# Performance work log

Measured on AMD Instinct MI355X. Metric: run time of the kernel, lower is better.

The kernel has to match this reference:

```python
import jax, jax.numpy as jnp
import numpy as np

L, B, S, D, N, H = 4, 4, 1024, 1024, 64, 16   # layers, batch, seq, d_model, d_state, heads
DI = 2 * D      # d_inner (expand_factor=2)
DH = D // H     # head dim
DF = 4 * D      # ffn hidden
SCALE = 1.0 / np.sqrt(DH)


def setup_inputs() -> dict:
    key = jax.random.key(0)
    ks = jax.random.split(key, 12)
    w = lambda k, sh: jax.random.normal(k, sh, jnp.float32) * 0.02
    return {
        "x": jax.random.normal(ks[0], (B, S, D), jnp.float32),
        "A_log": jax.random.normal(ks[1], (L, N), jnp.float32),
        "Dp": jax.random.normal(ks[2], (L, D), jnp.float32),
        "W_in": w(ks[3], (L, 2 * DI, D)), "b_in": jnp.zeros((L, 2 * DI), jnp.float32),
        "W_xp": w(ks[4], (L, N, DI)), "b_xp": jnp.zeros((L, N), jnp.float32),
        "W_dt": w(ks[5], (L, D, DI)), "b_dt": jnp.zeros((L, D), jnp.float32),
        "W_out": w(ks[6], (L, D, DI)), "b_out": jnp.zeros((L, D), jnp.float32),
        "W_qkv": w(ks[7], (L, 3 * D, D)), "b_qkv": jnp.zeros((L, 3 * D), jnp.float32),
        "W_ao": w(ks[8], (L, D, D)), "b_ao": jnp.zeros((L, D), jnp.float32),
        "g1": jnp.ones((L, D), jnp.float32), "be1": jnp.zeros((L, D), jnp.float32),
        "g2": jnp.ones((L, D), jnp.float32), "be2": jnp.zeros((L, D), jnp.float32),
        "W_f1": w(ks[9], (L, DF, D)), "b_f1": jnp.zeros((L, DF), jnp.float32),
        "W_f2": w(ks[10], (L, D, DF)), "b_f2": jnp.zeros((L, D), jnp.float32),
    }


def _ln(x, g, b, eps=1e-5):
    mu = x.mean(-1, keepdims=True)
    var = ((x - mu) ** 2).mean(-1, keepdims=True)
    return (x - mu) * jax.lax.rsqrt(var + eps) * g + b


def _mamba(x, A_log, Dp, W_in, b_in, W_xp, b_xp, W_dt, b_dt, W_out, b_out):
    xr = jnp.einsum('bsd,od->bso', x, W_in) + b_in          # [b,s,2*DI]
    xi, res = jnp.split(xr, 2, axis=-1)
    xi = jax.nn.silu(xi)
    A = -jnp.exp(A_log)                                      # [N]
    delta = jax.nn.softplus(jnp.einsum('bsi,di->bsd', xi, W_dt) + b_dt)  # [b,s,D]
    m = delta.mean(-1)                                       # [b,s]
    A_disc = jnp.exp(A[None, None, :] * m[:, :, None])       # [b,s,N]
    u = jnp.einsum('bsi,ni->bsn', xi, W_xp) + b_xp           # [b,s,N]

    def step(state, inp):
        a_t, u_t = inp
        state = a_t * state + u_t                            # [b,N]
        return state, state.sum(-1)                          # carry, emit sum over d_state

    init = jnp.zeros((x.shape[0], A_log.shape[0]), x.dtype)
    _, ssum = jax.lax.scan(step, init, (A_disc.swapaxes(0, 1), u.swapaxes(0, 1)))
    ssum = ssum.swapaxes(0, 1)                               # [b,s]
    y = ssum[..., None] * xi                                 # [b,s,DI]
    y = y * jax.nn.silu(res)
    y = jnp.einsum('bsi,di->bsd', y, W_out) + b_out
    return y + x * Dp


def _attn(x, W_qkv, b_qkv, W_ao, b_ao):
    b, s, d = x.shape
    qkv = jnp.einsum('bsd,od->bso', x, W_qkv) + b_qkv        # [b,s,3d]
    qkv = qkv.reshape(b, s, 3, H, DH)
    q = jnp.moveaxis(qkv[:, :, 0], 2, 1)                     # [b,h,s,dh]
    k = jnp.moveaxis(qkv[:, :, 1], 2, 1)
    v = jnp.moveaxis(qkv[:, :, 2], 2, 1)
    scores = jnp.einsum('bhqd,bhkd->bhqk', q, k) * SCALE
    wts = jax.nn.softmax(scores, axis=-1)
    o = jnp.einsum('bhqk,bhkd->bhqd', wts, v)
    o = jnp.moveaxis(o, 1, 2).reshape(b, s, d)
    return jnp.einsum('bsd,od->bso', o, W_ao) + b_ao


def _forward(x, A_log, Dp, W_in, b_in, W_xp, b_xp, W_dt, b_dt, W_out, b_out,
             W_qkv, b_qkv, W_ao, b_ao, g1, be1, g2, be2, W_f1, b_f1, W_f2, b_f2):
    for l in range(L):
        m = _mamba(x, A_log[l], Dp[l], W_in[l], b_in[l], W_xp[l], b_xp[l],
                   W_dt[l], b_dt[l], W_out[l], b_out[l])
        x = _ln(x + m, g1[l], be1[l])
        a = _attn(x, W_qkv[l], b_qkv[l], W_ao[l], b_ao[l])
        x = _ln(x + a, g2[l], be2[l])
        h = jax.nn.gelu(jnp.einsum('bsd,fd->bsf', x, W_f1[l]) + b_f1[l], approximate=False)
        x = x + jnp.einsum('bsf,df->bsd', h, W_f2[l]) + b_f2[l]
    return x


def reference(x, A_log, Dp, W_in, b_in, W_xp, b_xp, W_dt, b_dt, W_out, b_out,
              W_qkv, b_qkv, W_ao, b_ao, g1, be1, g2, be2, W_f1, b_f1, W_f2, b_f2):
    return _forward(x, A_log, Dp, W_in, b_in, W_xp, b_xp, W_dt, b_dt, W_out, b_out,
                    W_qkv, b_qkv, W_ao, b_ao, g1, be1, g2, be2, W_f1, b_f1, W_f2, b_f2)
```

## Files before the change

kernel.cpp:

```cpp
#include <hip/hip_runtime.h>
#include <math.h>

typedef unsigned short ushort_t;
typedef unsigned int uint_t;
typedef __attribute__((ext_vector_type(8))) short short8;
typedef __attribute__((ext_vector_type(4))) float f32x4;

constexpr int Bb = 4, Ss = 1024, Dd = 1024, Nn = 64, Hh = 16;
constexpr int DIi = 2048, DFf = 4096;
constexpr int TOKENS = Bb * Ss;

constexpr size_t O_IN  = 0;
constexpr size_t O_DT  = 4194304;
constexpr size_t O_XP  = O_DT + 2097152;
constexpr size_t O_OUT = O_XP + 262144;
constexpr size_t O_QKV = O_OUT + 2097152;
constexpr size_t O_AO  = O_QKV + 3145728;
constexpr size_t O_F1  = O_AO + 1048576;
constexpr size_t O_F2  = O_F1 + 4194304;
constexpr size_t W_TOTAL = O_F2 + 4194304;
constexpr size_t W_QUADS = W_TOTAL / 4;

enum { EPI_SPLIT = 0, EPI_B16, EPI_GELU, EPI_DTXP, EPI_DP, EPI_F32, EPI_RESID };

__device__ __forceinline__ float siluf(float x) { return x / (1.f + expf(-x)); }
__device__ __forceinline__ float softplusf(float x) { return fmaxf(x, 0.f) + log1pf(expf(-fabsf(x))); }
__device__ __forceinline__ float geluf(float x) { return 0.5f * x * (1.f + erff(x * 0.7071067811865476f)); }

__device__ __forceinline__ float bf2f(uint_t u) {
    union { uint_t i; float f; } v; v.i = u << 16; return v.f;
}
__device__ __forceinline__ ushort_t f2bf(float f) {
    union { float f; uint_t i; } v; v.f = f;
    return (ushort_t)((v.i + 0x7FFFu + ((v.i >> 16) & 1u)) >> 16);
}

__device__ __forceinline__ void gload_lds16(const ushort_t* g, ushort_t* l) {
    __builtin_amdgcn_global_load_lds(
        (const __attribute__((address_space(1))) unsigned int*)g,
        (__attribute__((address_space(3))) unsigned int*)l, 16, 0, 0);
}

template <int EPI>
__global__ __launch_bounds__(256) void gemm_mfma(
    const ushort_t* __restrict__ A, const ushort_t* __restrict__ Bw,
    const float* __restrict__ bias, int M, int N, int K,
    float* __restrict__ of0, float* __restrict__ of1,
    ushort_t* __restrict__ ob0, ushort_t* __restrict__ ob1,
    const float* __restrict__ e0, const float* __restrict__ e1)
{
    __shared__ __attribute__((aligned(16))) ushort_t AB[24576];
    const int tid = threadIdx.x;
    const int lane = tid & 63, wid = tid >> 6;
    const int wr = wid >> 1, wc = wid & 1;
    const int l15 = lane & 15, lg = lane >> 4;

    int bx = blockIdx.x, by = blockIdx.y;
    const int gx = gridDim.x;
    if ((gx & 7) == 0) {
        const int s = by * gx + bx;
        const int xcd = s & 7, c = s >> 3;
        const int cpx = gx >> 3;
        bx = xcd * cpx + (c % cpx);
        by = c / cpx;
    }
    const int m0 = by << 7, n0 = bx << 7;

    f32x4 acc[4][4];
#pragma unroll
    for (int i = 0; i < 4; ++i)
#pragma unroll
        for (int j = 0; j < 4; ++j) { acc[i][j][0] = 0.f; acc[i][j][1] = 0.f; acc[i][j][2] = 0.f; acc[i][j][3] = 0.f; }

    const int srow4 = lane >> 2;
    const int scc4  = (lane & 3) ^ ((lane >> 3) & 3);
    const ushort_t* Ag = A + (size_t)(m0 + wid * 32 + srow4) * K + scc4 * 8;
    const ushort_t* Bg = Bw + (size_t)(n0 + wid * 32 + srow4) * K + scc4 * 8;

#define STAGE_(b_, k0_)                                                          \
    {                                                                            \
        ushort_t* d_ = AB + (b_) * 8192;                                         \
        gload_lds16(Ag + (k0_),                  d_ + (wid * 32) * 32);          \
        gload_lds16(Ag + (size_t)16 * K + (k0_), d_ + (wid * 32 + 16) * 32);     \
        gload_lds16(Bg + (k0_),                  d_ + 4096 + (wid * 32) * 32);   \
        gload_lds16(Bg + (size_t)16 * K + (k0_), d_ + 4096 + (wid * 32 + 16) * 32); \
    }

    const int NS = K >> 5;
    STAGE_(0, 0);
    STAGE_(1, 32);
    asm volatile("s_waitcnt vmcnt(4)" ::: "memory");
    __builtin_amdgcn_s_barrier();

    const int chAB = (lg ^ ((l15 >> 1) & 3)) * 8;
    int bc = 0, bp = 2;
    for (int s = 0; s < NS; ++s) {
        if (s + 2 < NS) STAGE_(bp, (s + 2) << 5);
        const ushort_t* As_ = AB + bc * 8192;
        const ushort_t* Bs_ = As_ + 4096;
        short8 af[4], bfr[4];
#pragma unroll
        for (int mi = 0; mi < 4; ++mi)
            af[mi] = *(const short8*)&As_[(wr * 64 + mi * 16 + l15) * 32 + chAB];
#pragma unroll
        for (int nj = 0; nj < 4; ++nj)
            bfr[nj] = *(const short8*)&Bs_[(wc * 64 + nj * 16 + l15) * 32 + chAB];
#pragma unroll
        for (int mi = 0; mi < 4; ++mi)
#pragma unroll
            for (int nj = 0; nj < 4; ++nj)
                acc[mi][nj] = __builtin_amdgcn_mfma_f32_16x16x32_bf16(
                    af[mi], bfr[nj], acc[mi][nj], 0, 0, 0);
        if (s + 1 < NS) {
            if (s + 2 < NS) asm volatile("s_waitcnt vmcnt(4)" ::: "memory");
            else            asm volatile("s_waitcnt vmcnt(0)" ::: "memory");
            __builtin_amdgcn_s_barrier();
        }
        bc = (bc == 2) ? 0 : bc + 1;
        bp = (bp == 2) ? 0 : bp + 1;
    }
#undef STAGE_
    __syncthreads();

    if (EPI == EPI_SPLIT || EPI == EPI_B16 || EPI == EPI_GELU) {
        const bool lo = (EPI != EPI_SPLIT) || (n0 < DIi);
#pragma unroll
        for (int nj = 0; nj < 4; ++nj) {
            const int coll = wc * 64 + nj * 16 + l15;
            const float bv = bias[n0 + coll];
#pragma unroll
            for (int mi = 0; mi < 4; ++mi)
#pragma unroll
                for (int r = 0; r < 4; ++r) {
                    float v = acc[mi][nj][r] + bv;
                    if (EPI == EPI_SPLIT) v = lo ? siluf(v) : v;
                    else if (EPI == EPI_GELU) v = geluf(v);
                    AB[(wr * 64 + mi * 16 + lg * 4 + r) * 128 + coll] = f2bf(v);
                }
        }
        __syncthreads();
        ushort_t* dst = (EPI == EPI_SPLIT) ? (lo ? ob0 : ob1) : ob0;
        const int Nd = (EPI == EPI_SPLIT) ? DIi : N;
        const int nb = (EPI == EPI_SPLIT && !lo) ? (n0 - DIi) : n0;
#pragma unroll
        for (int i = 0; i < 8; ++i) {
            const int c = i * 256 + tid;
            const int row = c >> 4, ch = c & 15;
            *(uint4*)&dst[(size_t)(m0 + row) * Nd + nb + ch * 8] =
                *(const uint4*)&AB[row * 128 + ch * 8];
        }
    } else {
        float* Cf = (float*)AB;
#pragma unroll
        for (int pass = 0; pass < 2; ++pass) {
            if (pass) __syncthreads();
            if (wr == pass) {
#pragma unroll
                for (int nj = 0; nj < 4; ++nj) {
                    const int coll = wc * 64 + nj * 16 + l15;
                    const float bv = bias[n0 + coll];
#pragma unroll
                    for (int mi = 0; mi < 4; ++mi)
#pragma unroll
                        for (int r = 0; r < 4; ++r)
                            Cf[(mi * 16 + lg * 4 + r) * 128 + coll] = acc[mi][nj][r] + bv;
                }
            }
            __syncthreads();
#pragma unroll
            for (int i = 0; i < 8; ++i) {
                const int c = i * 256 + tid;
                const int row = c >> 5, ch = c & 31;
                const int grow = m0 + pass * 64 + row;
                const int gcol = n0 + ch * 4;
                float4 v = *(const float4*)&Cf[row * 128 + ch * 4];
                if (EPI == EPI_DTXP) {
                    if (n0 < Dd) {
                        v.x = softplusf(v.x); v.y = softplusf(v.y);
                        v.z = softplusf(v.z); v.w = softplusf(v.w);
                        *(float4*)&of0[(size_t)grow * Dd + gcol] = v;
                    } else {
                        *(float4*)&of1[(size_t)grow * 128 + (gcol - Dd)] = v;
                    }
                } else if (EPI == EPI_DP) {
                    const float4 e = *(const float4*)&e0[(size_t)grow * N + gcol];
                    const float4 d = *(const float4*)&e1[gcol];
                    v.x = fmaf(e.x, d.x, v.x); v.y = fmaf(e.y, d.y, v.y);
                    v.z = fmaf(e.z, d.z, v.z); v.w = fmaf(e.w, d.w, v.w);
                    *(float4*)&of0[(size_t)grow * N + gcol] = v;
                } else if (EPI == EPI_F32) {
                    *(float4*)&of0[(size_t)grow * N + gcol] = v;
                } else {
                    const float4 e = *(const float4*)&e0[(size_t)grow * N + gcol];
                    v.x += e.x; v.y += e.y; v.z += e.z; v.w += e.w;
                    *(float4*)&of0[(size_t)grow * N + gcol] = v;
                    uint2 w;
                    w.x = (uint_t)f2bf(v.x) | ((uint_t)f2bf(v.y) << 16);
                    w.y = (uint_t)f2bf(v.z) | ((uint_t)f2bf(v.w) << 16);
                    *(uint2*)&ob0[(size_t)grow * N + gcol] = w;
                }
            }
        }
    }
}

__global__ __launch_bounds__(256) void convert_weights_kernel(
    const float* __restrict__ Win, const float* __restrict__ Wdt,
    const float* __restrict__ Wxp, const float* __restrict__ Wout,
    const float* __restrict__ Wqkv, const float* __restrict__ Wao,
    const float* __restrict__ Wf1, const float* __restrict__ Wf2,
    const float* __restrict__ bdt, const float* __restrict__ bxp,
    ushort_t* __restrict__ dst, float* __restrict__ bcat)
{
    size_t q = (size_t)blockIdx.x * blockDim.x + threadIdx.x;
    if (q < 288) {
#pragma unroll
        for (int j = 0; j < 4; ++j) {
            const int e = (int)q * 4 + j;
            bcat[e] = (e < Dd) ? bdt[e] : ((e < Dd + Nn) ? bxp[e - Dd] : 0.f);
        }
    }
    const size_t stride = (size_t)gridDim.x * blockDim.x;
    for (; q < W_QUADS; q += stride) {
        const size_t e = q * 4;
        float4 v;
        if (e < O_DT)       v = *(const float4*)&Win[e - O_IN];
        else if (e < O_XP)  v = *(const float4*)&Wdt[e - O_DT];
        else if (e < O_OUT) {
            const size_t li = e - O_XP;
            const int row = (int)(li >> 11), colq = (int)(li & 2047);
            v = (row < Nn) ? *(const float4*)&Wxp[(size_t)row * DIi + colq]
                           : make_float4(0.f, 0.f, 0.f, 0.f);
        }
        else if (e < O_QKV) v = *(const float4*)&Wout[e - O_OUT];
        else if (e < O_AO)  v = *(const float4*)&Wqkv[e - O_QKV];
        else if (e < O_F1)  v = *(const float4*)&Wao[e - O_AO];
        else if (e < O_F2)  v = *(const float4*)&Wf1[e - O_F1];
        else                v = *(const float4*)&Wf2[e - O_F2];
        uint2 w;
        w.x = (uint_t)f2bf(v.x) | ((uint_t)f2bf(v.y) << 16);
        w.y = (uint_t)f2bf(v.z) | ((uint_t)f2bf(v.w) << 16);
        *(uint2*)&dst[e] = w;
    }
}

__global__ __launch_bounds__(256) void cvt_f32_bf16_kernel(
    const float* __restrict__ in, ushort_t* __restrict__ out)
{
    const size_t i4 = (size_t)blockIdx.x * blockDim.x + threadIdx.x;
    const float4 v = *(const float4*)&in[i4 * 4];
    uint2 w;
    w.x = (uint_t)f2bf(v.x) | ((uint_t)f2bf(v.y) << 16);
    w.y = (uint_t)f2bf(v.z) | ((uint_t)f2bf(v.w) << 16);
    *(uint2*)&out[i4 * 4] = w;
}

__global__ __launch_bounds__(256) void row_mean_kernel(const float* __restrict__ in,
                                                       float* __restrict__ out)
{
    __shared__ float red[4];
    const int tid = threadIdx.x;
    const size_t base = (size_t)blockIdx.x * Dd;
    const float4 v = *(const float4*)&in[base + tid * 4];
    float s = v.x + v.y + v.z + v.w;
#pragma unroll
    for (int off = 32; off; off >>= 1) s += __shfl_xor(s, off);
    if ((tid & 63) == 0) red[tid >> 6] = s;
    __syncthreads();
    if (tid == 0) out[blockIdx.x] = (red[0] + red[1] + red[2] + red[3]) * (1.f / (float)Dd);
}

__global__ __launch_bounds__(256) void ln_residual_kernel(
    float* __restrict__ xio, const float* __restrict__ addin,
    const float* __restrict__ g, const float* __restrict__ be,
    ushort_t* __restrict__ xb)
{
    __shared__ float red[8];
    const int tid = threadIdx.x;
    const size_t base = (size_t)blockIdx.x * Dd;
    const float4 xv = *(const float4*)&xio[base + tid * 4];
    const float4 av = *(const float4*)&addin[base + tid * 4];
    float v[4] = {xv.x + av.x, xv.y + av.y, xv.z + av.z, xv.w + av.w};
    float s = v[0] + v[1] + v[2] + v[3];
    float s2 = v[0] * v[0] + v[1] * v[1] + v[2] * v[2] + v[3] * v[3];
#pragma unroll
    for (int off = 32; off; off >>= 1) { s += __shfl_xor(s, off); s2 += __shfl_xor(s2, off); }
    if ((tid & 63) == 0) { red[tid >> 6] = s; red[4 + (tid >> 6)] = s2; }
    __syncthreads();
    const float mu = (red[0] + red[1] + red[2] + red[3]) * (1.f / (float)Dd);
    const float var = (red[4] + red[5] + red[6] + red[7]) * (1.f / (float)Dd) - mu * mu;
    const float rstd = rsqrtf(var + 1e-5f);
    const float4 gv = *(const float4*)&g[tid * 4];
    const float4 bv = *(const float4*)&be[tid * 4];
    float o[4];
    o[0] = (v[0] - mu) * rstd * gv.x + bv.x;
    o[1] = (v[1] - mu) * rstd * gv.y + bv.y;
    o[2] = (v[2] - mu) * rstd * gv.z + bv.z;
    o[3] = (v[3] - mu) * rstd * gv.w + bv.w;
    *(float4*)&xio[base + tid * 4] = make_float4(o[0], o[1], o[2], o[3]);
    uint2 w;
    w.x = (uint_t)f2bf(o[0]) | ((uint_t)f2bf(o[1]) << 16);
    w.y = (uint_t)f2bf(o[2]) | ((uint_t)f2bf(o[3]) << 16);
    *(uint2*)&xb[base + tid * 4] = w;
}

__global__ __launch_bounds__(1024) void scan_fused_kernel(
    const float* __restrict__ A_log_l, const float* __restrict__ m,
    const float* __restrict__ u, float* __restrict__ ssum)
{
    __shared__ float Ps[16][64];
    __shared__ float Sl[16][64];
    __shared__ float Cs[16][64];
    const int b = blockIdx.x;
    const int tid = threadIdx.x;
    const int n = tid & 63, c = tid >> 6;
    const int t0 = b * Ss + c * 64;
    const float Aval = -expf(A_log_l[n]);

    float S = 0.f, msum = 0.f;
#pragma unroll 8
    for (int t = 0; t < 64; ++t) {
        const float mt = m[t0 + t];
        msum += mt;
        S = fmaf(expf(Aval * mt), S, u[(size_t)(t0 + t) * 128 + n]);
    }
    Ps[c][n] = expf(Aval * msum);
    Sl[c][n] = S;
    __syncthreads();

    if (c == 0) {
        float carry = 0.f;
#pragma unroll
        for (int cc = 0; cc < 16; ++cc) {
            Cs[cc][n] = carry;
            carry = fmaf(Ps[cc][n], carry, Sl[cc][n]);
        }
    }
    __syncthreads();

    float st = Cs[c][n];
#pragma unroll 4
    for (int t = 0; t < 64; ++t) {
        st = fmaf(expf(Aval * m[t0 + t]), st, u[(size_t)(t0 + t) * 128 + n]);
        float r = st;
#pragma unroll
        for (int off = 32; off; off >>= 1) r += __shfl_xor(r, off);
        if (n == 0) ssum[t0 + t] = r;
    }
}

__global__ __launch_bounds__(256) void y_gate_kernel(
    ushort_t* __restrict__ xi, const ushort_t* __restrict__ res,
    const float* __restrict__ ssum)
{
    const size_t i8 = (size_t)blockIdx.x * blockDim.x + threadIdx.x;
    const int t = (int)(i8 >> 8);
    const float sv = ssum[t];
    uint4 xw = *(const uint4*)&xi[i8 * 8];
    const uint4 rw = *(const uint4*)&res[i8 * 8];
    const uint_t xs[4] = {xw.x, xw.y, xw.z, xw.w};
    const uint_t rs[4] = {rw.x, rw.y, rw.z, rw.w};
    uint_t os[4];
#pragma unroll
    for (int j = 0; j < 4; ++j) {
        const float x0 = bf2f(xs[j] & 0xffffu), x1 = bf2f(xs[j] >> 16);
        const float r0 = bf2f(rs[j] & 0xffffu), r1 = bf2f(rs[j] >> 16);
        os[j] = (uint_t)f2bf(sv * x0 * siluf(r0)) | ((uint_t)f2bf(sv * x1 * siluf(r1)) << 16);
    }
    *(uint4*)&xi[i8 * 8] = make_uint4(os[0], os[1], os[2], os[3]);
}

__global__ __launch_bounds__(256) void transpose_v_kernel(
    const ushort_t* __restrict__ qkv, ushort_t* __restrict__ vt)
{
    __shared__ ushort_t T[64][68];
    const int b = blockIdx.z, h = blockIdx.y, st = blockIdx.x;
    const int tid = threadIdx.x;
    const int sl = tid >> 3, d0 = (tid & 7) * 8;
#pragma unroll
    for (int it = 0; it < 2; ++it) {
        const int s = sl + it * 32;
        const uint4 w = *(const uint4*)&qkv[(size_t)(b * Ss + st * 64 + s) * 3072 + 2048 + h * 64 + d0];
        *(uint2*)&T[s][d0]     = make_uint2(w.x, w.y);
        *(uint2*)&T[s][d0 + 4] = make_uint2(w.z, w.w);
    }
    __syncthreads();
    const int dl = tid >> 3, s0 = (tid & 7) * 8;
#pragma unroll
    for (int it = 0; it < 2; ++it) {
        const int d = dl + it * 32;
        uint_t w[4];
#pragma unroll
        for (int j = 0; j < 4; ++j)
            w[j] = (uint_t)T[s0 + 2 * j][d] | ((uint_t)T[s0 + 2 * j + 1][d] << 16);
        *(uint4*)&vt[(size_t)((b * Hh + h) * 64 + d) * Ss + st * 64 + s0] =
            make_uint4(w[0], w[1], w[2], w[3]);
    }
}

__global__ __launch_bounds__(256) void attn_mfma_kernel(
    const ushort_t* __restrict__ qkv, const ushort_t* __restrict__ vt,
    ushort_t* __restrict__ out)
{
    __shared__ ushort_t Ks[64 * 64];
    __shared__ ushort_t Vs[64 * 64];
    __shared__ __attribute__((aligned(16))) ushort_t Pb[4][2560];

    const int tid = threadIdx.x;
    const int lane = tid & 63, wid = tid >> 6;
    const int b = blockIdx.z, h = blockIdx.y;
    const int q0 = blockIdx.x * 128 + wid * 32;
    const int l15 = lane & 15, lg = lane >> 4;
    constexpr float CEXP = 0.125f * 1.44269504f;

    short8 qf[2][2];
#pragma unroll
    for (int mi = 0; mi < 2; ++mi)
#pragma unroll
        for (int kk = 0; kk < 2; ++kk)
            qf[mi][kk] = *(const short8*)&qkv[(size_t)(b * Ss + q0 + mi * 16 + l15) * 3072
                                              + h * 64 + kk * 32 + lg * 8];

    f32x4 oacc[2][4];
#pragma unroll
    for (int mi = 0; mi < 2; ++mi)
#pragma unroll
        for (int nj = 0; nj < 4; ++nj) { oacc[mi][nj][0]=0.f; oacc[mi][nj][1]=0.f; oacc[mi][nj][2]=0.f; oacc[mi][nj][3]=0.f; }
    float lrun[2][4];
#pragma unroll
    for (int mi = 0; mi < 2; ++mi)
#pragma unroll
        for (int r = 0; r < 4; ++r) lrun[mi][r] = 0.f;

    const int srow = lane >> 3;
    const int scc  = (lane & 7) ^ srow;
    const ushort_t* Kg = qkv + (size_t)(b * Ss + wid * 16 + srow) * 3072 + 1024 + h * 64 + scc * 8;
    const ushort_t* Vg = vt + (size_t)((b * Hh + h) * 64 + wid * 16 + srow) * Ss + scc * 8;

    for (int kt = 0; kt < Ss / 64; ++kt) {
#pragma unroll
        for (int j = 0; j < 2; ++j) {
            gload_lds16(Kg + (size_t)(kt * 64 + j * 8) * 3072, Ks + (wid * 16 + j * 8) * 64);
            gload_lds16(Vg + (size_t)j * 8 * Ss + kt * 64,     Vs + (wid * 16 + j * 8) * 64);
        }
        __syncthreads();

        f32x4 sacc[2][4];
#pragma unroll
        for (int mi = 0; mi < 2; ++mi)
#pragma unroll
            for (int nj = 0; nj < 4; ++nj) { sacc[mi][nj][0]=0.f; sacc[mi][nj][1]=0.f; sacc[mi][nj][2]=0.f; sacc[mi][nj][3]=0.f; }
#pragma unroll
        for (int kk = 0; kk < 2; ++kk) {
            short8 kf[4];
#pragma unroll
            for (int nj = 0; nj < 4; ++nj) {
                const int row = nj * 16 + l15;
                const int ch = (kk * 4 + lg) ^ (row & 7);
                kf[nj] = *(const short8*)&Ks[row * 64 + ch * 8];
            }
#pragma unroll
            for (int mi = 0; mi < 2; ++mi)
#pragma unroll
                for (int nj = 0; nj < 4; ++nj)
                    sacc[mi][nj] = __builtin_amdgcn_mfma_f32_16x16x32_bf16(
                        qf[mi][kk], kf[nj], sacc[mi][nj], 0, 0, 0);
        }

#pragma unroll
        for (int mi = 0; mi < 2; ++mi)
#pragma unroll
            for (int nj = 0; nj < 4; ++nj) {
                const int bi = mi * 2 + (nj >> 1);
                const int chsw = ((nj & 1) * 2 + (l15 >> 3)) ^ lg;
#pragma unroll
                for (int r = 0; r < 4; ++r) {
                    const float p = exp2f(sacc[mi][nj][r] * CEXP);
                    lrun[mi][r] += p;
                    const int q15 = lg * 4 + r;
                    Pb[wid][bi * 640 + q15 * 40 + chsw * 8 + (lane & 7)] = f2bf(p);
                }
            }

#pragma unroll
        for (int kk = 0; kk < 2; ++kk) {
            short8 pa[2], vb[4];
#pragma unroll
            for (int mi = 0; mi < 2; ++mi) {
                const int chsw = lg ^ (l15 >> 2);
                pa[mi] = *(const short8*)&Pb[wid][(mi * 2 + kk) * 640 + l15 * 40 + chsw * 8];
            }
#pragma unroll
            for (int nj = 0; nj < 4; ++nj) {
                const int row = nj * 16 + l15;
                const int ch = (kk * 4 + lg) ^ (row & 7);
                vb[nj] = *(const short8*)&Vs[row * 64 + ch * 8];
            }
#pragma unroll
            for (int mi = 0; mi < 2; ++mi)
#pragma unroll
                for (int nj = 0; nj < 4; ++nj)
                    oacc[mi][nj] = __builtin_amdgcn_mfma_f32_16x16x32_bf16(
                        pa[mi], vb[nj], oacc[mi][nj], 0, 0, 0);
        }
        __syncthreads();
    }

#pragma unroll
    for (int mi = 0; mi < 2; ++mi)
#pragma unroll
        for (int r = 0; r < 4; ++r) {
            float s = lrun[mi][r];
#pragma unroll
            for (int off = 1; off < 16; off <<= 1) s += __shfl_xor(s, off);
            lrun[mi][r] = 1.f / s;
        }
#pragma unroll
    for (int mi = 0; mi < 2; ++mi)
#pragma unroll
        for (int r = 0; r < 4; ++r) {
            const int q = q0 + mi * 16 + lg * 4 + r;
            const float inv = lrun[mi][r];
#pragma unroll
            for (int nj = 0; nj < 4; ++nj)
                out[(size_t)(b * Ss + q) * Dd + h * 64 + nj * 16 + l15] =
                    f2bf(oacc[mi][nj][r] * inv);
        }
}

extern "C" void kernel_launch(void* const* d_in, const int* in_sizes, int n_in,
                              void* d_out, int out_size, void* d_ws, size_t ws_size,
                              hipStream_t stream)
{
    const float* x_in  = (const float*)d_in[0];
    const float* A_log = (const float*)d_in[1];
    const float* Dp    = (const float*)d_in[2];
    const float* W_in  = (const float*)d_in[3];
    const float* b_in  = (const float*)d_in[4];
    const float* W_xp  = (const float*)d_in[5];
    const float* b_xp  = (const float*)d_in[6];
    const float* W_dt  = (const float*)d_in[7];
    const float* b_dt  = (const float*)d_in[8];
    const float* W_out = (const float*)d_in[9];
    const float* b_out = (const float*)d_in[10];
    const float* W_qkv = (const float*)d_in[11];
    const float* b_qkv = (const float*)d_in[12];
    const float* W_ao  = (const float*)d_in[13];
    const float* b_ao  = (const float*)d_in[14];
    const float* g1    = (const float*)d_in[15];
    const float* be1   = (const float*)d_in[16];
    const float* g2    = (const float*)d_in[17];
    const float* be2   = (const float*)d_in[18];
    const float* W_f1  = (const float*)d_in[19];
    const float* b_f1  = (const float*)d_in[20];
    const float* W_f2  = (const float*)d_in[21];
    const float* b_f2  = (const float*)d_in[22];

    float* xf      = (float*)d_ws;
    float* a3      = xf + 4194304;
    float* ub      = a3 + 4194304;
    float* mb      = ub + 524288;
    float* sb      = mb + 4096;
    float* bcat    = sb + 4096;
    ushort_t* xb    = (ushort_t*)(bcat + 1152);
    ushort_t* xi_b  = xb + 4194304;
    ushort_t* res_b = xi_b + 8388608;
    ushort_t* qh_b  = res_b + 8388608;
    ushort_t* ao_b  = qh_b + 16777216;
    ushort_t* Wb    = ao_b + 4194304;
    ushort_t* vt_b  = Wb + W_TOTAL;

    hipMemcpyAsync(xf, x_in, (size_t)TOKENS * Dd * sizeof(float),
                   hipMemcpyDeviceToDevice, stream);
    cvt_f32_bf16_kernel<<<dim3(4096), dim3(256), 0, stream>>>(x_in, xb);

    const dim3 blk(256);

    for (int l = 0; l < 4; ++l) {
        convert_weights_kernel<<<dim3(2048), blk, 0, stream>>>(
            W_in + (size_t)l * 4194304, W_dt + (size_t)l * 2097152,
            W_xp + (size_t)l * 131072,  W_out + (size_t)l * 2097152,
            W_qkv + (size_t)l * 3145728, W_ao + (size_t)l * 1048576,
            W_f1 + (size_t)l * 4194304, W_f2 + (size_t)l * 4194304,
            b_dt + (size_t)l * 1024, b_xp + (size_t)l * Nn, Wb, bcat);

        gemm_mfma<EPI_SPLIT><<<dim3(32, 32), blk, 0, stream>>>(
            xb, Wb + O_IN, b_in + (size_t)l * 4096, TOKENS, 4096, 1024,
            nullptr, nullptr, xi_b, res_b, nullptr, nullptr);
        gemm_mfma<EPI_DTXP><<<dim3(9, 32), blk, 0, stream>>>(
            xi_b, Wb + O_DT, bcat, TOKENS, 1152, 2048,
            a3, ub, nullptr, nullptr, nullptr, nullptr);
        row_mean_kernel<<<dim3(TOKENS), blk, 0, stream>>>(a3, mb);
        scan_fused_kernel<<<dim3(Bb), dim3(1024), 0, stream>>>(
            A_log + (size_t)l * Nn, mb, ub, sb);
        y_gate_kernel<<<dim3(4096), blk, 0, stream>>>(xi_b, res_b, sb);
        gemm_mfma<EPI_DP><<<dim3(8, 32), blk, 0, stream>>>(
            xi_b, Wb + O_OUT, b_out + (size_t)l * 1024, TOKENS, 1024, 2048,
            a3, nullptr, nullptr, nullptr, xf, Dp + (size_t)l * 1024);
        ln_residual_kernel<<<dim3(TOKENS), blk, 0, stream>>>(
            xf, a3, g1 + (size_t)l * 1024, be1 + (size_t)l * 1024, xb);
        gemm_mfma<EPI_B16><<<dim3(24, 32), blk, 0, stream>>>(
            xb, Wb + O_QKV, b_qkv + (size_t)l * 3072, TOKENS, 3072, 1024,
            nullptr, nullptr, qh_b, nullptr, nullptr, nullptr);
        transpose_v_kernel<<<dim3(16, Hh, Bb), blk, 0, stream>>>(qh_b, vt_b);
        attn_mfma_kernel<<<dim3(8, Hh, Bb), blk, 0, stream>>>(qh_b, vt_b, ao_b);
        gemm_mfma<EPI_F32><<<dim3(8, 32), blk, 0, stream>>>(
            ao_b, Wb + O_AO, b_ao + (size_t)l * 1024, TOKENS, 1024, 1024,
            a3, nullptr, nullptr, nullptr, nullptr, nullptr);
        ln_residual_kernel<<<dim3(TOKENS), blk, 0, stream>>>(
            xf, a3, g2 + (size_t)l * 1024, be2 + (size_t)l * 1024, xb);
        gemm_mfma<EPI_GELU><<<dim3(32, 32), blk, 0, stream>>>(
            xb, Wb + O_F1, b_f1 + (size_t)l * 4096, TOKENS, 4096, 1024,
            nullptr, nullptr, qh_b, nullptr, nullptr, nullptr);
        gemm_mfma<EPI_RESID><<<dim3(8, 32), blk, 0, stream>>>(
            qh_b, Wb + O_F2, b_f2 + (size_t)l * 1024, TOKENS, 1024, 4096,
            xf, nullptr, xb, nullptr, xf, nullptr);
    }

    hipMemcpyAsync(d_out, xf, (size_t)TOKENS * Dd * sizeof(float),
                   hipMemcpyDeviceToDevice, stream);
    (void)in_sizes; (void)n_in; (void)out_size; (void)ws_size;
}
```

Measured before the change: 1.890 ms.

## Add 64-row GEMM tiles for narrow outputs and deepen LDS pipeline

Templates the GEMM on an M tile size and a buffer count. The narrow-N GEMMs (dt/xp, out-proj, attn-out, FFN2) switch to 64x128 tiles with 4 waves side by side along N, which doubles grid size from 256-288 blocks so the many CUs on the chip stay busy. Most GEMMs also move from a 3-buffer to a 4-buffer global-to-LDS prefetch with a generalized vmcnt wait. The smaller tiles cut data reuse per block, and the deeper buffering raises LDS use, which may lower occupancy.

```diff
diff --git a/kernel.cpp b/kernel.cpp
--- a/kernel.cpp
+++ b/kernel.cpp
@@ -41,7 +41,15 @@
         (__attribute__((address_space(3))) unsigned int*)l, 16, 0, 0);
 }
 
-template <int EPI>
+__device__ __forceinline__ void wait_vm(int n) {
+    if (n == 0)      asm volatile("s_waitcnt vmcnt(0)" ::: "memory");
+    else if (n == 3) asm volatile("s_waitcnt vmcnt(3)" ::: "memory");
+    else if (n == 4) asm volatile("s_waitcnt vmcnt(4)" ::: "memory");
+    else if (n == 6) asm volatile("s_waitcnt vmcnt(6)" ::: "memory");
+    else             asm volatile("s_waitcnt vmcnt(8)" ::: "memory");
+}
+
+template <int EPI, int MT, int NBUF>
 __global__ __launch_bounds__(256) void gemm_mfma(
     const ushort_t* __restrict__ A, const ushort_t* __restrict__ Bw,
     const float* __restrict__ bias, int M, int N, int K,
@@ -49,10 +57,16 @@
     ushort_t* __restrict__ ob0, ushort_t* __restrict__ ob1,
     const float* __restrict__ e0, const float* __restrict__ e1)
 {
-    __shared__ __attribute__((aligned(16))) ushort_t AB[24576];
+    constexpr int BUFSZ = (MT == 128) ? 8192 : 6144;
+    constexpr int DEPTH = NBUF - 1;
+    constexpr int L     = (MT == 128) ? 4 : 3;
+    constexpr int NJ    = (MT == 128) ? 4 : 2;
+    __shared__ __attribute__((aligned(16))) ushort_t AB[NBUF * BUFSZ];
+
     const int tid = threadIdx.x;
     const int lane = tid & 63, wid = tid >> 6;
-    const int wr = wid >> 1, wc = wid & 1;
+    const int wr = (MT == 128) ? (wid >> 1) : 0;
+    const int wc = (MT == 128) ? (wid & 1) : wid;
     const int l15 = lane & 15, lg = lane >> 4;
 
     int bx = blockIdx.x, by = blockIdx.y;
@@ -64,65 +78,82 @@
         bx = xcd * cpx + (c % cpx);
         by = c / cpx;
     }
-    const int m0 = by << 7, n0 = bx << 7;
-
-    f32x4 acc[4][4];
+    const int m0 = by * MT, n0 = bx << 7;
+
+    f32x4 acc[4][NJ];
 #pragma unroll
     for (int i = 0; i < 4; ++i)
 #pragma unroll
-        for (int j = 0; j < 4; ++j) { acc[i][j][0] = 0.f; acc[i][j][1] = 0.f; acc[i][j][2] = 0.f; acc[i][j][3] = 0.f; }
+        for (int j = 0; j < NJ; ++j) { acc[i][j][0] = 0.f; acc[i][j][1] = 0.f; acc[i][j][2] = 0.f; acc[i][j][3] = 0.f; }
 
     const int srow4 = lane >> 2;
     const int scc4  = (lane & 3) ^ ((lane >> 3) & 3);
     const ushort_t* Ag = A + (size_t)(m0 + wid * 32 + srow4) * K + scc4 * 8;
     const ushort_t* Bg = Bw + (size_t)(n0 + wid * 32 + srow4) * K + scc4 * 8;
-
-#define STAGE_(b_, k0_)                                                          \
-    {                                                                            \
-        ushort_t* d_ = AB + (b_) * 8192;                                         \
-        gload_lds16(Ag + (k0_),                  d_ + (wid * 32) * 32);          \
-        gload_lds16(Ag + (size_t)16 * K + (k0_), d_ + (wid * 32 + 16) * 32);     \
-        gload_lds16(Bg + (k0_),                  d_ + 4096 + (wid * 32) * 32);   \
-        gload_lds16(Bg + (size_t)16 * K + (k0_), d_ + 4096 + (wid * 32 + 16) * 32); \
-    }
+    const ushort_t* sb64[3];
+    int do64[3];
+    if (MT == 64) {
+#pragma unroll
+        for (int j = 0; j < 3; ++j) {
+            const int i = wid * 3 + j;
+            const bool isA = i < 4;
+            const int rb = (isA ? i : i - 4) * 16;
+            sb64[j] = (isA ? A + (size_t)(m0 + rb + srow4) * K
+                           : Bw + (size_t)(n0 + rb + srow4) * K) + scc4 * 8;
+            do64[j] = (isA ? 0 : 2048) + rb * 32;
+        }
+    }
+
+    auto STAGE = [&](int b_, int k0_) {
+        ushort_t* d_ = AB + b_ * BUFSZ;
+        if constexpr (MT == 128) {
+            gload_lds16(Ag + k0_,                  d_ + (wid * 32) * 32);
+            gload_lds16(Ag + (size_t)16 * K + k0_, d_ + (wid * 32 + 16) * 32);
+            gload_lds16(Bg + k0_,                  d_ + 4096 + (wid * 32) * 32);
+            gload_lds16(Bg + (size_t)16 * K + k0_, d_ + 4096 + (wid * 32 + 16) * 32);
+        } else {
+#pragma unroll
+            for (int j = 0; j < 3; ++j)
+                gload_lds16(sb64[j] + k0_, d_ + do64[j]);
+        }
+    };
 
     const int NS = K >> 5;
-    STAGE_(0, 0);
-    STAGE_(1, 32);
-    asm volatile("s_waitcnt vmcnt(4)" ::: "memory");
+#pragma unroll
+    for (int p = 0; p < DEPTH; ++p) STAGE(p, p * 32);
+    wait_vm((DEPTH - 1) * L);
     __builtin_amdgcn_s_barrier();
 
     const int chAB = (lg ^ ((l15 >> 1) & 3)) * 8;
-    int bc = 0, bp = 2;
+    int bc = 0, bp = DEPTH;
     for (int s = 0; s < NS; ++s) {
-        if (s + 2 < NS) STAGE_(bp, (s + 2) << 5);
-        const ushort_t* As_ = AB + bc * 8192;
-        const ushort_t* Bs_ = As_ + 4096;
-        short8 af[4], bfr[4];
+        if (s + DEPTH < NS) STAGE(bp, (s + DEPTH) << 5);
+        const ushort_t* As_ = AB + bc * BUFSZ;
+        const ushort_t* Bs_ = As_ + ((MT == 128) ? 4096 : 2048);
+        short8 af[4], bfr[NJ];
 #pragma unroll
         for (int mi = 0; mi < 4; ++mi)
             af[mi] = *(const short8*)&As_[(wr * 64 + mi * 16 + l15) * 32 + chAB];
 #pragma unroll
-        for (int nj = 0; nj < 4; ++nj)
-            bfr[nj] = *(const short8*)&Bs_[(wc * 64 + nj * 16 + l15) * 32 + chAB];
+        for (int nj = 0; nj < NJ; ++nj)
+            bfr[nj] = *(const short8*)&Bs_[(wc * (MT == 128 ? 64 : 32) + nj * 16 + l15) * 32 + chAB];
 #pragma unroll
         for (int mi = 0; mi < 4; ++mi)
 #pragma unroll
-            for (int nj = 0; nj < 4; ++nj)
+            for (int nj = 0; nj < NJ; ++nj)
                 acc[mi][nj] = __builtin_amdgcn_mfma_f32_16x16x32_bf16(
                     af[mi], bfr[nj], acc[mi][nj], 0, 0, 0);
         if (s + 1 < NS) {
-            if (s + 2 < NS) asm volatile("s_waitcnt vmcnt(4)" ::: "memory");
-            else            asm volatile("s_waitcnt vmcnt(0)" ::: "memory");
+            const int rem = NS - 2 - s;
+            wait_vm(((rem < DEPTH - 1) ? rem : DEPTH - 1) * L);
             __builtin_amdgcn_s_barrier();
         }
-        bc = (bc == 2) ? 0 : bc + 1;
-        bp = (bp == 2) ? 0 : bp + 1;
-    }
-#undef STAGE_
+        bc = (bc + 1 == NBUF) ? 0 : bc + 1;
+        bp = (bp + 1 == NBUF) ? 0 : bp + 1;
+    }
     __syncthreads();
 
-    if (EPI == EPI_SPLIT || EPI == EPI_B16 || EPI == EPI_GELU) {
+    if constexpr (MT == 128) {
         const bool lo = (EPI != EPI_SPLIT) || (n0 < DIi);
 #pragma unroll
         for (int nj = 0; nj < 4; ++nj) {
@@ -152,53 +183,47 @@
     } else {
         float* Cf = (float*)AB;
 #pragma unroll
-        for (int pass = 0; pass < 2; ++pass) {
-            if (pass) __syncthreads();
-            if (wr == pass) {
-#pragma unroll
-                for (int nj = 0; nj < 4; ++nj) {
-                    const int coll = wc * 64 + nj * 16 + l15;
-                    const float bv = bias[n0 + coll];
-#pragma unroll
-                    for (int mi = 0; mi < 4; ++mi)
-#pragma unroll
-                        for (int r = 0; r < 4; ++r)
-                            Cf[(mi * 16 + lg * 4 + r) * 128 + coll] = acc[mi][nj][r] + bv;
+        for (int nj = 0; nj < NJ; ++nj) {
+            const int coll = wc * 32 + nj * 16 + l15;
+            const float bv = bias[n0 + coll];
+#pragma unroll
+            for (int mi = 0; mi < 4; ++mi)
+#pragma unroll
+                for (int r = 0; r < 4; ++r)
+                    Cf[(mi * 16 + lg * 4 + r) * 128 + coll] = acc[mi][nj][r] + bv;
+        }
+        __syncthreads();
+#pragma unroll
+        for (int i = 0; i < 8; ++i) {
+            const int c = i * 256 + tid;
+            const int row = c >> 5, ch = c & 31;
+            const int grow = m0 + row;
+            const int gcol = n0 + ch * 4;
+            float4 v = *(const float4*)&Cf[row * 128 + ch * 4];
+            if (EPI == EPI_DTXP) {
+                if (n0 < Dd) {
+                    v.x = softplusf(v.x); v.y = softplusf(v.y);
+                    v.z = softplusf(v.z); v.w = softplusf(v.w);
+                    *(float4*)&of0[(size_t)grow * Dd + gcol] = v;
+                } else {
+                    *(float4*)&of1[(size_t)grow * 128 + (gcol - Dd)] = v;
                 }
-            }
-            __syncthreads();
-#pragma unroll
-            for (int i = 0; i < 8; ++i) {
-                const int c = i * 256 + tid;
-                const int row = c >> 5, ch = c & 31;
-                const int grow = m0 + pass * 64 + row;
-                const int gcol = n0 + ch * 4;
-                float4 v = *(const float4*)&Cf[row * 128 + ch * 4];
-                if (EPI == EPI_DTXP) {
-                    if (n0 < Dd) {
-                        v.x = softplusf(v.x); v.y = softplusf(v.y);
-                        v.z = softplusf(v.z); v.w = softplusf(v.w);
-                        *(float4*)&of0[(size_t)grow * Dd + gcol] = v;
-                    } else {
-                        *(float4*)&of1[(size_t)grow * 128 + (gcol - Dd)] = v;
-                    }
-                } else if (EPI == EPI_DP) {
-                    const float4 e = *(const float4*)&e0[(size_t)grow * N + gcol];
-                    const float4 d = *(const float4*)&e1[gcol];
-                    v.x = fmaf(e.x, d.x, v.x); v.y = fmaf(e.y, d.y, v.y);
-                    v.z = fmaf(e.z, d.z, v.z); v.w = fmaf(e.w, d.w, v.w);
-                    *(float4*)&of0[(size_t)grow * N + gcol] = v;
-                } else if (EPI == EPI_F32) {
-                    *(float4*)&of0[(size_t)grow * N + gcol] = v;
-                } else {
-                    const float4 e = *(const float4*)&e0[(size_t)grow * N + gcol];
-                    v.x += e.x; v.y += e.y; v.z += e.z; v.w += e.w;
-                    *(float4*)&of0[(size_t)grow * N + gcol] = v;
-                    uint2 w;
-                    w.x = (uint_t)f2bf(v.x) | ((uint_t)f2bf(v.y) << 16);
-                    w.y = (uint_t)f2bf(v.z) | ((uint_t)f2bf(v.w) << 16);
-                    *(uint2*)&ob0[(size_t)grow * N + gcol] = w;
-                }
+            } else if (EPI == EPI_DP) {
+                const float4 e = *(const float4*)&e0[(size_t)grow * N + gcol];
+                const float4 d = *(const float4*)&e1[gcol];
+                v.x = fmaf(e.x, d.x, v.x); v.y = fmaf(e.y, d.y, v.y);
+                v.z = fmaf(e.z, d.z, v.z); v.w = fmaf(e.w, d.w, v.w);
+                *(float4*)&of0[(size_t)grow * N + gcol] = v;
+            } else if (EPI == EPI_F32) {
+                *(float4*)&of0[(size_t)grow * N + gcol] = v;
+            } else {
+                const float4 e = *(const float4*)&e0[(size_t)grow * N + gcol];
+                v.x += e.x; v.y += e.y; v.z += e.z; v.w += e.w;
+                *(float4*)&of0[(size_t)grow * N + gcol] = v;
+                uint2 w;
+                w.x = (uint_t)f2bf(v.x) | ((uint_t)f2bf(v.y) << 16);
+                w.y = (uint_t)f2bf(v.z) | ((uint_t)f2bf(v.w) << 16);
+                *(uint2*)&ob0[(size_t)grow * N + gcol] = w;
             }
         }
     }
@@ -584,35 +609,35 @@
             W_f1 + (size_t)l * 4194304, W_f2 + (size_t)l * 4194304,
             b_dt + (size_t)l * 1024, b_xp + (size_t)l * Nn, Wb, bcat);
 
-        gemm_mfma<EPI_SPLIT><<<dim3(32, 32), blk, 0, stream>>>(
+        gemm_mfma<EPI_SPLIT, 128, 4><<<dim3(32, 32), blk, 0, stream>>>(
             xb, Wb + O_IN, b_in + (size_t)l * 4096, TOKENS, 4096, 1024,
             nullptr, nullptr, xi_b, res_b, nullptr, nullptr);
-        gemm_mfma<EPI_DTXP><<<dim3(9, 32), blk, 0, stream>>>(
+        gemm_mfma<EPI_DTXP, 64, 4><<<dim3(9, 64), blk, 0, stream>>>(
             xi_b, Wb + O_DT, bcat, TOKENS, 1152, 2048,
             a3, ub, nullptr, nullptr, nullptr, nullptr);
         row_mean_kernel<<<dim3(TOKENS), blk, 0, stream>>>(a3, mb);
         scan_fused_kernel<<<dim3(Bb), dim3(1024), 0, stream>>>(
             A_log + (size_t)l * Nn, mb, ub, sb);
         y_gate_kernel<<<dim3(4096), blk, 0, stream>>>(xi_b, res_b, sb);
-        gemm_mfma<EPI_DP><<<dim3(8, 32), blk, 0, stream>>>(
+        gemm_mfma<EPI_DP, 64, 4><<<dim3(8, 64), blk, 0, stream>>>(
             xi_b, Wb + O_OUT, b_out + (size_t)l * 1024, TOKENS, 1024, 2048,
             a3, nullptr, nullptr, nullptr, xf, Dp + (size_t)l * 1024);
         ln_residual_kernel<<<dim3(TOKENS), blk, 0, stream>>>(
             xf, a3, g1 + (size_t)l * 1024, be1 + (size_t)l * 1024, xb);
-        gemm_mfma<EPI_B16><<<dim3(24, 32), blk, 0, stream>>>(
+        gemm_mfma<EPI_B16, 128, 3><<<dim3(24, 32), blk, 0, stream>>>(
             xb, Wb + O_QKV, b_qkv + (size_t)l * 3072, TOKENS, 3072, 1024,
             nullptr, nullptr, qh_b, nullptr, nullptr, nullptr);
         transpose_v_kernel<<<dim3(16, Hh, Bb), blk, 0, stream>>>(qh_b, vt_b);
         attn_mfma_kernel<<<dim3(8, Hh, Bb), blk, 0, stream>>>(qh_b, vt_b, ao_b);
-        gemm_mfma<EPI_F32><<<dim3(8, 32), blk, 0, stream>>>(
+        gemm_mfma<EPI_F32, 64, 4><<<dim3(8, 64), blk, 0, stream>>>(
             ao_b, Wb + O_AO, b_ao + (size_t)l * 1024, TOKENS, 1024, 1024,
             a3, nullptr, nullptr, nullptr, nullptr, nullptr);
         ln_residual_kernel<<<dim3(TOKENS), blk, 0, stream>>>(
             xf, a3, g2 + (size_t)l * 1024, be2 + (size_t)l * 1024, xb);
-        gemm_mfma<EPI_GELU><<<dim3(32, 32), blk, 0, stream>>>(
+        gemm_mfma<EPI_GELU, 128, 4><<<dim3(32, 32), blk, 0, stream>>>(
             xb, Wb + O_F1, b_f1 + (size_t)l * 4096, TOKENS, 4096, 1024,
             nullptr, nullptr, qh_b, nullptr, nullptr, nullptr);
-        gemm_mfma<EPI_RESID><<<dim3(8, 32), blk, 0, stream>>>(
+        gemm_mfma<EPI_RESID, 64, 4><<<dim3(8, 64), blk, 0, stream>>>(
             qh_b, Wb + O_F2, b_f2 + (size_t)l * 1024, TOKENS, 1024, 4096,
             xf, nullptr, xb, nullptr, xf, nullptr);
     }
```

After: 1.919 ms. Within noise of the previous version (+1.5%).
